# Kernel tuning notes

Hardware: AMD Instinct MI355X
Metric: run time of the kernel (lower is better)

Reference implementation:

```python
import jax, jax.numpy as jnp
import numpy as np

B, S, F, H, D = 32, 512, 32, 8, 300   # batch, seq, n_features, hidden_dim, n_dim_model
FH = min(D, F)                        # flattened GRN hidden = min(n_dim_model, n_features)


def _p(key, shape, scale=0.05):
    return (jax.random.normal(key, shape) * scale).astype(jnp.float32)


def setup_inputs() -> dict:
    key = jax.random.key(0)
    ks = jax.random.split(key, 16)
    return {
        "x": jax.random.normal(ks[0], (B, S, F), dtype=jnp.float32),
        "pre_w": _p(ks[1], (F, H)), "pre_b": _p(ks[2], (F, H)),
        "sg_fc1_w": _p(ks[3], (F, H, H)), "sg_fc1_b": _p(ks[4], (F, H)),
        "sg_fc2_w": _p(ks[5], (F, H, D)), "sg_fc2_b": _p(ks[6], (F, D)),
        "sg_gate_w": _p(ks[7], (F, D, 2 * D)), "sg_gate_b": _p(ks[8], (F, 2 * D)),
        "sg_ln_g": jnp.ones((F, D), jnp.float32), "sg_ln_b": jnp.zeros((F, D), jnp.float32),
        "fl_fc1_w": _p(ks[9], (F * H, FH)), "fl_fc1_b": _p(ks[10], (FH,)),
        "fl_fc2_w": _p(ks[11], (FH, F)), "fl_fc2_b": _p(ks[12], (F,)),
        "fl_gate_w": _p(ks[13], (F, 2 * F)), "fl_gate_b": _p(ks[14], (2 * F,)),
        "fl_ln_g": jnp.ones((F,), jnp.float32), "fl_ln_b": jnp.zeros((F,), jnp.float32),
    }


def _interp_last(x, out_dim):
    # torch F.interpolate(mode='linear', align_corners=True) along the last axis
    in_dim = x.shape[-1]
    pos = jnp.arange(out_dim) * ((in_dim - 1) / (out_dim - 1))
    lo = jnp.floor(pos).astype(jnp.int32)
    hi = jnp.minimum(lo + 1, in_dim - 1)
    w = (pos - lo.astype(pos.dtype)).astype(x.dtype)
    return x[..., lo] * (1 - w) + x[..., hi] * w


def _layer_norm(x, g, b, eps=1e-5):
    m = jnp.mean(x, axis=-1, keepdims=True)
    v = jnp.var(x, axis=-1, keepdims=True)
    return (x - m) * jax.lax.rsqrt(v + eps) * g + b


def _forward(x, pre_w, pre_b, sg_fc1_w, sg_fc1_b, sg_fc2_w, sg_fc2_b,
             sg_gate_w, sg_gate_b, sg_ln_g, sg_ln_b,
             fl_fc1_w, fl_fc1_b, fl_fc2_w, fl_fc2_b, fl_gate_w, fl_gate_b,
             fl_ln_g, fl_ln_b):
    # per-feature prescaler: Linear(1, H) for each of F features, batched
    pre = x[..., None] * pre_w + pre_b                                   # [B,S,F,H]

    # per-feature GRN (H -> H -> D), batched over the feature axis f
    h = jax.nn.elu(jnp.einsum('bsfh,fhk->bsfk', pre, sg_fc1_w) + sg_fc1_b)
    h = jnp.einsum('bsfk,fkd->bsfd', h, sg_fc2_w) + sg_fc2_b             # [B,S,F,D]
    g = jnp.einsum('bsfd,fdp->bsfp', h, sg_gate_w) + sg_gate_b           # [B,S,F,2D]
    glu = g[..., :D] * jax.nn.sigmoid(g[..., D:])
    residual = _interp_last(pre, D)                                      # H -> D interpolate projection
    outputs = _layer_norm(glu + residual, sg_ln_g, sg_ln_b)              # [B,S,F,D]

    # flattened GRN on concatenated prescaler outputs (F*H -> FH -> F)
    flat = pre.reshape(pre.shape[0], pre.shape[1], F * H)                # matches torch.cat order
    fh = jax.nn.elu(flat @ fl_fc1_w + fl_fc1_b)
    fh = fh @ fl_fc2_w + fl_fc2_b                                        # [B,S,F]
    fg = fh @ fl_gate_w + fl_gate_b                                      # [B,S,2F]
    fglu = fg[..., :F] * jax.nn.sigmoid(fg[..., F:])
    wlogits = _layer_norm(fglu + _interp_last(flat, F), fl_ln_g, fl_ln_b)
    w = jax.nn.softmax(wlogits, axis=-1)                                 # [B,S,F]

    out = jnp.einsum('bsfd,bsf->bsd', outputs, w)                        # softmax-weighted sum over features
    return out, w[..., None, :]                                          # weights unsqueezed at dim -2


def reference(x, pre_w, pre_b, sg_fc1_w, sg_fc1_b, sg_fc2_w, sg_fc2_b,
              sg_gate_w, sg_gate_b, sg_ln_g, sg_ln_b,
              fl_fc1_w, fl_fc1_b, fl_fc2_w, fl_fc2_b, fl_gate_w, fl_gate_b,
              fl_ln_g, fl_ln_b):
    return _forward(x, pre_w, pre_b, sg_fc1_w, sg_fc1_b, sg_fc2_w, sg_fc2_b,
                    sg_gate_w, sg_gate_b, sg_ln_g, sg_ln_b,
                    fl_fc1_w, fl_fc1_b, fl_fc2_w, fl_fc2_b, fl_gate_w, fl_gate_b,
                    fl_ln_g, fl_ln_b)
```

## Files before the change

### kernel.cpp

```cpp
#include <hip/hip_runtime.h>
#include <hip/hip_bf16.h>

#define NB 32
#define NS 512
#define NF 32
#define NH 8
#define ND 300
#define NTOK (NB*NS)
#define TPW 8
#define WPB 2
#define TPB (TPW*WPB)

#define L2E 1.4426950408889634f

using bf16 = __hip_bfloat16;
typedef float v2f __attribute__((ext_vector_type(2)));

__device__ __forceinline__ float rcpf_(float x){ return __builtin_amdgcn_rcpf(x); }
__device__ __forceinline__ float rsqf_(float x){ return __builtin_amdgcn_rsqf(x); }
__device__ __forceinline__ float sigm(float x){ return rcpf_(1.0f + __expf(-x)); }
__device__ __forceinline__ float sigm2(float x){ return rcpf_(1.0f + __builtin_amdgcn_exp2f(-x)); }
__device__ __forceinline__ float eluf(float x){ return x > 0.0f ? x : __expf(x) - 1.0f; }

__device__ __forceinline__ v2f fma2(v2f a, v2f b, v2f c){
    return __builtin_elementwise_fma(a, b, c);
}
__device__ __forceinline__ v2f fma2s(float s, v2f b, v2f c){
    return __builtin_elementwise_fma((v2f){s, s}, b, c);
}

template<int BF16>
__device__ __forceinline__ float ldf(const void* p, size_t i){
    if (BF16) return __bfloat162float(((const bf16*)p)[i]);
    return ((const float*)p)[i];
}
template<int BF16>
__device__ __forceinline__ void stf(void* p, size_t i, float v){
    if (BF16) ((bf16*)p)[i] = __float2bfloat16(v);
    else      ((float*)p)[i] = v;
}

__device__ __forceinline__ bool is_bf16(const void* ones){
    return *(const unsigned*)ones == 0x3F803F80u;
}

__device__ __forceinline__ v2f unpk(unsigned u){
    return (v2f){ __int_as_float((int)(u << 16)),
                  __int_as_float((int)(u & 0xFFFF0000u)) };
}
__device__ __forceinline__ unsigned pack_bf(float a, float b){
    bf16 ha = __float2bfloat16(a), hb = __float2bfloat16(b);
    return (unsigned)*(unsigned short*)&ha | ((unsigned)*(unsigned short*)&hb << 16);
}

template<int CTRL>
__device__ __forceinline__ float dppadd(float v){
    return v + __int_as_float(__builtin_amdgcn_update_dpp(
        0, __float_as_int(v), CTRL, 0xF, 0xF, true));
}
template<int CTRL>
__device__ __forceinline__ float dppmax(float v){
    return fmaxf(v, __int_as_float(__builtin_amdgcn_update_dpp(
        __float_as_int(v), __float_as_int(v), CTRL, 0xF, 0xF, false)));
}
__device__ __forceinline__ float rlane(float v, int l){
    return __int_as_float(__builtin_amdgcn_readlane(__float_as_int(v), l));
}
__device__ __forceinline__ float wsum64(float v){
    v = dppadd<0x111>(v); v = dppadd<0x112>(v); v = dppadd<0x114>(v); v = dppadd<0x118>(v);
    v = dppadd<0x142>(v); v = dppadd<0x143>(v);
    return rlane(v, 63);
}
__device__ __forceinline__ float rsum32(float v){
    v = dppadd<0x111>(v); v = dppadd<0x112>(v); v = dppadd<0x114>(v); v = dppadd<0x118>(v);
    return rlane(v, 15) + rlane(v, 31);
}
__device__ __forceinline__ float rmax32(float v){
    v = dppmax<0x111>(v); v = dppmax<0x112>(v); v = dppmax<0x114>(v); v = dppmax<0x118>(v);
    return fmaxf(rlane(v, 15), rlane(v, 31));
}

template<int BF16>
__device__ void precompute_body(const void* __restrict__ W2, const void* __restrict__ b2,
                                const void* __restrict__ Wg, const void* __restrict__ bg,
                                const void* __restrict__ sg_g, const void* __restrict__ sg_b,
                                unsigned* __restrict__ Crow,
                                float* __restrict__ w2t, float* __restrict__ b2s,
                                float (*part)[64][18])
{
    const int tid  = threadIdx.x;
    const int lane = tid & 63;
    const int wv   = tid >> 6;
    const int f    = blockIdx.x & 31;
    const int c    = blockIdx.x >> 5;
    const int d    = c * 64 + lane;
    const int dc   = d < 299 ? d : 299;

    for (int idx = tid; idx < 2400; idx += 512) {
        int m = idx >> 3, k = idx & 7;
        w2t[idx] = ldf<BF16>(W2, (size_t)f * 2400 + (size_t)k * 300 + m);
    }
    if (tid < 300) b2s[tid] = ldf<BF16>(b2, (size_t)f * 300 + tid);
    __syncthreads();

    v2f aA01 = {0,0}, aA23 = {0,0}, aA45 = {0,0}, aA67 = {0,0};
    v2f aB01 = {0,0}, aB23 = {0,0}, aB45 = {0,0}, aB67 = {0,0};
    float bAa = 0.f, bBa = 0.f;

    const int m0 = (wv * 300) >> 3;
    const int m1 = ((wv + 1) * 300) >> 3;
    const size_t WgF = (size_t)f * 180000 + dc;
    #pragma unroll 4
    for (int m = m0; m < m1; ++m) {
        float wa = ldf<BF16>(Wg, WgF + (size_t)m * 600);
        float wb = ldf<BF16>(Wg, WgF + (size_t)m * 600 + 300);
        float4 wk0 = *(const float4*)(w2t + m * 8);
        float4 wk1 = *(const float4*)(w2t + m * 8 + 4);
        aA01 = fma2s(wa, (v2f){wk0.x, wk0.y}, aA01);
        aA23 = fma2s(wa, (v2f){wk0.z, wk0.w}, aA23);
        aA45 = fma2s(wa, (v2f){wk1.x, wk1.y}, aA45);
        aA67 = fma2s(wa, (v2f){wk1.z, wk1.w}, aA67);
        aB01 = fma2s(wb, (v2f){wk0.x, wk0.y}, aB01);
        aB23 = fma2s(wb, (v2f){wk0.z, wk0.w}, aB23);
        aB45 = fma2s(wb, (v2f){wk1.x, wk1.y}, aB45);
        aB67 = fma2s(wb, (v2f){wk1.z, wk1.w}, aB67);
        float b2v = b2s[m];
        bAa += b2v * wa;
        bBa += b2v * wb;
    }

    {
        float* p = part[wv][lane];
        p[0]  = aA01.x; p[1]  = aA01.y; p[2]  = aA23.x; p[3]  = aA23.y;
        p[4]  = aA45.x; p[5]  = aA45.y; p[6]  = aA67.x; p[7]  = aA67.y;
        p[8]  = aB01.x; p[9]  = aB01.y; p[10] = aB23.x; p[11] = aB23.y;
        p[12] = aB45.x; p[13] = aB45.y; p[14] = aB67.x; p[15] = aB67.y;
        p[16] = bAa;    p[17] = bBa;
    }
    __syncthreads();

    if (tid < 64 && d < 300) {
        float s[18];
        #pragma unroll
        for (int v = 0; v < 18; ++v) {
            float t0 = part[0][lane][v] + part[1][lane][v];
            float t1 = part[2][lane][v] + part[3][lane][v];
            float t2 = part[4][lane][v] + part[5][lane][v];
            float t3 = part[6][lane][v] + part[7][lane][v];
            s[v] = (t0 + t1) + (t2 + t3);
        }
        unsigned dw[12];
        #pragma unroll
        for (int k = 0; k < 8; ++k) dw[k] = pack_bf(s[k], s[8 + k] * L2E);
        dw[8]  = __float_as_uint(s[16] + ldf<BF16>(bg, (size_t)f * 600 + d));
        dw[9]  = __float_as_uint((s[17] + ldf<BF16>(bg, (size_t)f * 600 + d + 300)) * L2E);
        dw[10] = __float_as_uint(ldf<BF16>(sg_g, (size_t)f * 300 + d));
        dw[11] = __float_as_uint(ldf<BF16>(sg_b, (size_t)f * 300 + d));
        unsigned* row = Crow + (size_t)(f * 300 + d) * 12;
        *(uint4*)(row + 0) = make_uint4(dw[0], dw[1], dw[2],  dw[3]);
        *(uint4*)(row + 4) = make_uint4(dw[4], dw[5], dw[6],  dw[7]);
        *(uint4*)(row + 8) = make_uint4(dw[8], dw[9], dw[10], dw[11]);
    }
}

__global__ void precompute_kernel(const void* __restrict__ W2, const void* __restrict__ b2,
                                  const void* __restrict__ Wg, const void* __restrict__ bg,
                                  const void* __restrict__ sg_g, const void* __restrict__ sg_b,
                                  unsigned* __restrict__ Crow)
{
    __shared__ float w2t[2400];
    __shared__ float b2s[300];
    __shared__ float part[8][64][18];
    if (is_bf16(sg_g))
        precompute_body<1>(W2, b2, Wg, bg, sg_g, sg_b, Crow, w2t, b2s, part);
    else
        precompute_body<0>(W2, b2, Wg, bg, sg_g, sg_b, Crow, w2t, b2s, part);
}

template<int BF16>
__device__ void vsn_body(const void* __restrict__ x,
                         const void* __restrict__ pre_w, const void* __restrict__ pre_b,
                         const void* __restrict__ W1,    const void* __restrict__ b1,
                         const void* __restrict__ fl1w,  const void* __restrict__ fl1b,
                         const void* __restrict__ fl2w,  const void* __restrict__ fl2b,
                         const void* __restrict__ flgw,  const void* __restrict__ flgb,
                         const void* __restrict__ flng,  const void* __restrict__ flnb,
                         const unsigned* __restrict__ Crow,
                         void* __restrict__ d_out, float* preS_, unsigned* hS_)
{
    void* outMain = d_out;
    void* outW    = (char*)d_out + (size_t)NTOK * ND * (BF16 ? 2 : 4);

    const int tid  = threadIdx.x;
    const int wave = tid >> 6;
    const int lane = tid & 63;
    const int tokBase = blockIdx.x * TPB + wave * TPW;

    float*    myPre = preS_ + wave * (TPW * 256);
    unsigned* myH   = hS_   + wave * (TPW * 128);

    {
        float pw[4], pb[4];
        #pragma unroll
        for (int q = 0; q < 4; ++q) {
            pw[q] = ldf<BF16>(pre_w, 4 * lane + q);
            pb[q] = ldf<BF16>(pre_b, 4 * lane + q);
        }
        const int fidx = lane >> 1;
        #pragma unroll
        for (int t = 0; t < TPW; ++t) {
            float xv = ldf<BF16>(x, (size_t)(tokBase + t) * NF + fidx);
            float4 v;
            v.x = xv * pw[0] + pb[0];
            v.y = xv * pw[1] + pb[1];
            v.z = xv * pw[2] + pb[2];
            v.w = xv * pw[3] + pb[3];
            *(float4*)(&myPre[t * 256 + 4 * lane]) = v;
        }
    }

    {
        const int f  = lane >> 1;
        const int kh = (lane & 1) * 4;
        float w1r[8][4], b1r[4];
        #pragma unroll
        for (int m = 0; m < 8; ++m)
            #pragma unroll
            for (int q = 0; q < 4; ++q)
                w1r[m][q] = ldf<BF16>(W1, (size_t)(f * 8 + m) * 8 + kh + q);
        #pragma unroll
        for (int q = 0; q < 4; ++q) b1r[q] = ldf<BF16>(b1, f * 8 + kh + q);

        #pragma unroll
        for (int t = 0; t < TPW; ++t) {
            float pr[8];
            float4 pA = *(const float4*)(&myPre[t * 256 + f * 8]);
            float4 pB = *(const float4*)(&myPre[t * 256 + f * 8 + 4]);
            pr[0]=pA.x; pr[1]=pA.y; pr[2]=pA.z; pr[3]=pA.w;
            pr[4]=pB.x; pr[5]=pB.y; pr[6]=pB.z; pr[7]=pB.w;
            float a[4] = {b1r[0], b1r[1], b1r[2], b1r[3]};
            #pragma unroll
            for (int m = 0; m < 8; ++m)
                #pragma unroll
                for (int q = 0; q < 4; ++q)
                    a[q] += pr[m] * w1r[m][q];
            uint2 hp;
            hp.x = pack_bf(eluf(a[0]), eluf(a[1]));
            hp.y = pack_bf(eluf(a[2]), eluf(a[3]));
            *(uint2*)(&myH[t * 128 + 2 * lane]) = hp;
        }
    }

    const int jj = lane & 31;
    const int hB = lane >> 5;
    float wreg[TPW];
    {
        float f1b = (hB == 0) ? ldf<BF16>(fl1b, jj) : 0.0f;
        v2f p1v[TPW / 2];
        #pragma unroll
        for (int g = 0; g < TPW / 2; ++g) p1v[g] = (v2f){f1b, f1b};
        for (int kg = 0; kg < 32; ++kg) {
            const int kk = hB * 128 + kg * 4;
            float4 pr[TPW];
            #pragma unroll
            for (int t = 0; t < TPW; ++t)
                pr[t] = *(const float4*)(&myPre[t * 256 + kk]);
            float w0 = ldf<BF16>(fl1w, (size_t)(kk + 0) * 32 + jj);
            float w1 = ldf<BF16>(fl1w, (size_t)(kk + 1) * 32 + jj);
            float w2 = ldf<BF16>(fl1w, (size_t)(kk + 2) * 32 + jj);
            float w3 = ldf<BF16>(fl1w, (size_t)(kk + 3) * 32 + jj);
            #pragma unroll
            for (int g = 0; g < TPW / 2; ++g) {
                p1v[g] = fma2((v2f){pr[2*g].x, pr[2*g+1].x}, (v2f){w0, w0}, p1v[g]);
                p1v[g] = fma2((v2f){pr[2*g].y, pr[2*g+1].y}, (v2f){w1, w1}, p1v[g]);
                p1v[g] = fma2((v2f){pr[2*g].z, pr[2*g+1].z}, (v2f){w2, w2}, p1v[g]);
                p1v[g] = fma2((v2f){pr[2*g].w, pr[2*g+1].w}, (v2f){w3, w3}, p1v[g]);
            }
        }
        float fhv[TPW];
        #pragma unroll
        for (int t = 0; t < TPW; ++t) {
            float p1 = (t & 1) ? p1v[t >> 1].y : p1v[t >> 1].x;
            fhv[t] = eluf(p1 + __shfl_xor(p1, 32));
        }

        float p2[TPW];
        float f2b = ldf<BF16>(fl2b, jj);
        #pragma unroll
        for (int t = 0; t < TPW; ++t) p2[t] = f2b;
        #pragma unroll
        for (int k = 0; k < 32; ++k) {
            float wv = ldf<BF16>(fl2w, k * 32 + jj);
            #pragma unroll
            for (int t = 0; t < TPW; ++t) p2[t] += rlane(fhv[t], k) * wv;
        }
        float p3[TPW];
        float fgbv = ldf<BF16>(flgb, lane);
        #pragma unroll
        for (int t = 0; t < TPW; ++t) p3[t] = fgbv;
        #pragma unroll
        for (int k = 0; k < 32; ++k) {
            float wv = ldf<BF16>(flgw, k * 64 + lane);
            #pragma unroll
            for (int t = 0; t < TPW; ++t) p3[t] += rlane(p2[t], k) * wv;
        }

        float lng = ldf<BF16>(flng, jj), lnb = ldf<BF16>(flnb, jj);
        float posB = (float)jj * (255.0f / 31.0f);
        int loB = (int)floorf(posB); loB = loB < 0 ? 0 : (loB > 254 ? 254 : loB);
        float frB = posB - (float)loB;

        #pragma unroll
        for (int t = 0; t < TPW; ++t) {
            float fgA  = __shfl(p3[t], jj);
            float fgB  = __shfl(p3[t], jj + 32);
            float fglu = fgA * sigm(fgB);
            float pl = myPre[t * 256 + loB];
            float ph = myPre[t * 256 + loB + 1];
            float tv = fglu + pl + frB * (ph - pl);
            float S1 = rsum32(tv);
            float S2 = rsum32(tv * tv);
            float mean = S1 * (1.0f / 32.0f);
            float var  = fmaxf(S2 * (1.0f / 32.0f) - mean * mean, 0.0f);
            float rs   = rsqf_(var + 1e-5f);
            float wl   = (tv - mean) * rs * lng + lnb;
            float mx   = rmax32(wl);
            float e    = __expf(wl - mx);
            float ss   = rsum32(e);
            float wv   = e * rcpf_(ss);
            wreg[t] = wv;
            if (lane < 32) stf<BF16>(outW, (size_t)(tokBase + t) * NF + lane, wv);
        }
    }

    int lo_[5]; float fr_[5];
    #pragma unroll
    for (int i = 0; i < 5; ++i) {
        int d = i * 64 + lane;
        float pos = (float)d * (7.0f / 299.0f);
        int lo = (int)floorf(pos); lo = lo < 0 ? 0 : (lo > 6 ? 6 : lo);
        lo_[i] = lo; fr_[i] = pos - (float)lo;
    }

    float acc[TPW][5];
    #pragma unroll
    for (int t = 0; t < TPW; ++t)
        #pragma unroll
        for (int i = 0; i < 5; ++i) acc[t][i] = 0.0f;

    for (int f = 0; f < NF; ++f) {
        v2f  P[5][8];
        float bcA[5], bcB[5], lgv[5], lbv[5];
        #pragma unroll
        for (int i = 0; i < 5; ++i) {
            int d = i * 64 + lane;
            bool ok = (d < ND);
            const uint4* row = (const uint4*)(Crow + ((size_t)f * ND + (ok ? d : ND - 1)) * 12);
            uint4 c0 = row[0], c1 = row[1], c2 = row[2];
            P[i][0] = unpk(c0.x); P[i][1] = unpk(c0.y);
            P[i][2] = unpk(c0.z); P[i][3] = unpk(c0.w);
            P[i][4] = unpk(c1.x); P[i][5] = unpk(c1.y);
            P[i][6] = unpk(c1.z); P[i][7] = unpk(c1.w);
            bcA[i] = __uint_as_float(c2.x);
            bcB[i] = __uint_as_float(c2.y);
            lgv[i] = __uint_as_float(c2.z);
            lbv[i] = __uint_as_float(c2.w);
        }

        #pragma unroll
        for (int t = 0; t < TPW; ++t) {
            uint4 hp = *(const uint4*)(&myH[t * 128 + f * 4]);
            v2f h01 = unpk(hp.x), h23 = unpk(hp.y), h45 = unpk(hp.z), h67 = unpk(hp.w);

            float tt[5], a1 = 0.f, a2 = 0.f;
            #pragma unroll
            for (int i = 0; i < 5; ++i) {
                int d = i * 64 + lane;
                bool ok = (d < ND);
                v2f g = {bcA[i], bcB[i]};
                g = fma2s(h01.x, P[i][0], g);
                g = fma2s(h01.y, P[i][1], g);
                g = fma2s(h23.x, P[i][2], g);
                g = fma2s(h23.y, P[i][3], g);
                g = fma2s(h45.x, P[i][4], g);
                g = fma2s(h45.y, P[i][5], g);
                g = fma2s(h67.x, P[i][6], g);
                g = fma2s(h67.y, P[i][7], g);
                int base = f * 8 + lo_[i];
                float pl = myPre[t * 256 + base];
                float ph = myPre[t * 256 + base + 1];
                float tv = g.x * sigm2(g.y) + pl + fr_[i] * (ph - pl);
                tv = ok ? tv : 0.0f;
                tt[i] = tv; a1 += tv; a2 += tv * tv;
            }

            float S1 = wsum64(a1);
            float S2 = wsum64(a2);
            float mean = S1 * (1.0f / 300.0f);
            float var  = fmaxf(S2 * (1.0f / 300.0f) - mean * mean, 0.0f);
            float rs   = rsqf_(var + 1e-5f);
            float wf   = rlane(wreg[t], f);
            float c1v  = wf * rs;
            float c2v  = -c1v * mean;
            #pragma unroll
            for (int i = 0; i < 5; ++i) {
                int d = i * 64 + lane;
                if (d < ND) {
                    float v = fmaf(c1v, tt[i], c2v);
                    acc[t][i] = fmaf(lgv[i], v, fmaf(wf, lbv[i], acc[t][i]));
                }
            }
        }
    }

    #pragma unroll
    for (int t = 0; t < TPW; ++t) {
        const size_t tok = (size_t)tokBase + t;
        #pragma unroll
        for (int i = 0; i < 5; ++i) {
            int d = i * 64 + lane;
            if (d < ND) stf<BF16>(outMain, tok * ND + d, acc[t][i]);
        }
    }
}

__launch_bounds__(128)
__global__ void vsn_main(const void* __restrict__ x,
                         const void* __restrict__ pre_w, const void* __restrict__ pre_b,
                         const void* __restrict__ W1,    const void* __restrict__ b1,
                         const void* __restrict__ fl1w,  const void* __restrict__ fl1b,
                         const void* __restrict__ fl2w,  const void* __restrict__ fl2b,
                         const void* __restrict__ flgw,  const void* __restrict__ flgb,
                         const void* __restrict__ flng,  const void* __restrict__ flnb,
                         const unsigned* __restrict__ Crow, void* __restrict__ d_out)
{
    __shared__ float    preS_[WPB * TPW * 256];
    __shared__ unsigned hS_[WPB * TPW * 128];
    if (is_bf16(flng))
        vsn_body<1>(x, pre_w, pre_b, W1, b1, fl1w, fl1b, fl2w, fl2b,
                    flgw, flgb, flng, flnb, Crow, d_out, preS_, hS_);
    else
        vsn_body<0>(x, pre_w, pre_b, W1, b1, fl1w, fl1b, fl2w, fl2b,
                    flgw, flgb, flng, flnb, Crow, d_out, preS_, hS_);
}

extern "C" void kernel_launch(void* const* d_in, const int* in_sizes, int n_in,
                              void* d_out, int out_size, void* d_ws, size_t ws_size,
                              hipStream_t stream)
{
    const void* x     = d_in[0];
    const void* pre_w = d_in[1];
    const void* pre_b = d_in[2];
    const void* W1    = d_in[3];
    const void* b1    = d_in[4];
    const void* W2    = d_in[5];
    const void* b2    = d_in[6];
    const void* Wg    = d_in[7];
    const void* bg    = d_in[8];
    const void* sg_g  = d_in[9];
    const void* sg_b  = d_in[10];
    const void* fl1w  = d_in[11];
    const void* fl1b  = d_in[12];
    const void* fl2w  = d_in[13];
    const void* fl2b  = d_in[14];
    const void* flgw  = d_in[15];
    const void* flgb  = d_in[16];
    const void* flng  = d_in[17];
    const void* flnb  = d_in[18];

    unsigned* Crow = (unsigned*)d_ws;

    precompute_kernel<<<160, 512, 0, stream>>>(W2, b2, Wg, bg, sg_g, sg_b, Crow);

    vsn_main<<<NTOK / TPB, 128, 0, stream>>>(x, pre_w, pre_b, W1, b1,
        fl1w, fl1b, fl2w, fl2b, flgw, flgb, flng, flnb, Crow, d_out);
}
```

Before: 303.1 us.

## Split feature loop across waves per token block and precompute interpolated prescaler residual

Result: slower. 344.3 us (+13.6%).

```diff
diff --git a/kernel.cpp b/kernel.cpp
--- a/kernel.cpp
+++ b/kernel.cpp
@@ -9,7 +9,7 @@
 #define NTOK (NB*NS)
 #define TPW 8
 #define WPB 2
-#define TPB (TPW*WPB)
+#define TPB 8
 
 #define L2E 1.4426950408889634f
 
@@ -84,6 +84,7 @@
 __device__ void precompute_body(const void* __restrict__ W2, const void* __restrict__ b2,
                                 const void* __restrict__ Wg, const void* __restrict__ bg,
                                 const void* __restrict__ sg_g, const void* __restrict__ sg_b,
+                                const void* __restrict__ pre_w, const void* __restrict__ pre_b,
                                 unsigned* __restrict__ Crow,
                                 float* __restrict__ w2t, float* __restrict__ b2s,
                                 float (*part)[64][18])
@@ -156,25 +157,38 @@
         dw[9]  = __float_as_uint((s[17] + ldf<BF16>(bg, (size_t)f * 600 + d + 300)) * L2E);
         dw[10] = __float_as_uint(ldf<BF16>(sg_g, (size_t)f * 300 + d));
         dw[11] = __float_as_uint(ldf<BF16>(sg_b, (size_t)f * 300 + d));
-        unsigned* row = Crow + (size_t)(f * 300 + d) * 12;
-        *(uint4*)(row + 0) = make_uint4(dw[0], dw[1], dw[2],  dw[3]);
-        *(uint4*)(row + 4) = make_uint4(dw[4], dw[5], dw[6],  dw[7]);
-        *(uint4*)(row + 8) = make_uint4(dw[8], dw[9], dw[10], dw[11]);
+
+        float pos = (float)d * (7.0f / 299.0f);
+        int lo = (int)floorf(pos); lo = lo < 0 ? 0 : (lo > 6 ? 6 : lo);
+        float fr = pos - (float)lo;
+        float pwl = ldf<BF16>(pre_w, (size_t)f * 8 + lo);
+        float pwh = ldf<BF16>(pre_w, (size_t)f * 8 + lo + 1);
+        float pbl = ldf<BF16>(pre_b, (size_t)f * 8 + lo);
+        float pbh = ldf<BF16>(pre_b, (size_t)f * 8 + lo + 1);
+        unsigned rwu = __float_as_uint(pwl + fr * (pwh - pwl));
+        unsigned rbu = __float_as_uint(pbl + fr * (pbh - pbl));
+
+        unsigned* row = Crow + (size_t)(f * 300 + d) * 16;
+        *(uint4*)(row + 0)  = make_uint4(dw[0], dw[1], dw[2],  dw[3]);
+        *(uint4*)(row + 4)  = make_uint4(dw[4], dw[5], dw[6],  dw[7]);
+        *(uint4*)(row + 8)  = make_uint4(dw[8], dw[9], dw[10], dw[11]);
+        *(uint4*)(row + 12) = make_uint4(rwu, rbu, 0u, 0u);
     }
 }
 
 __global__ void precompute_kernel(const void* __restrict__ W2, const void* __restrict__ b2,
                                   const void* __restrict__ Wg, const void* __restrict__ bg,
                                   const void* __restrict__ sg_g, const void* __restrict__ sg_b,
+                                  const void* __restrict__ pre_w, const void* __restrict__ pre_b,
                                   unsigned* __restrict__ Crow)
 {
     __shared__ float w2t[2400];
     __shared__ float b2s[300];
     __shared__ float part[8][64][18];
     if (is_bf16(sg_g))
-        precompute_body<1>(W2, b2, Wg, bg, sg_g, sg_b, Crow, w2t, b2s, part);
+        precompute_body<1>(W2, b2, Wg, bg, sg_g, sg_b, pre_w, pre_b, Crow, w2t, b2s, part);
     else
-        precompute_body<0>(W2, b2, Wg, bg, sg_g, sg_b, Crow, w2t, b2s, part);
+        precompute_body<0>(W2, b2, Wg, bg, sg_g, sg_b, pre_w, pre_b, Crow, w2t, b2s, part);
 }
 
 template<int BF16>
@@ -186,18 +200,23 @@
                          const void* __restrict__ flgw,  const void* __restrict__ flgb,
                          const void* __restrict__ flng,  const void* __restrict__ flnb,
                          const unsigned* __restrict__ Crow,
-                         void* __restrict__ d_out, float* preS_, unsigned* hS_)
+                         void* __restrict__ d_out, float* preS, unsigned* hS)
 {
     void* outMain = d_out;
     void* outW    = (char*)d_out + (size_t)NTOK * ND * (BF16 ? 2 : 4);
 
-    const int tid  = threadIdx.x;
-    const int wave = tid >> 6;
-    const int lane = tid & 63;
-    const int tokBase = blockIdx.x * TPB + wave * TPW;
-
-    float*    myPre = preS_ + wave * (TPW * 256);
-    unsigned* myH   = hS_   + wave * (TPW * 128);
+    const int tid   = threadIdx.x;
+    const int wave  = tid >> 6;
+    const int lane  = tid & 63;
+    const int tokBase = blockIdx.x * TPB;
+    const int tA0   = wave * (TPB / WPB);
+    const int fBase = wave * (NF / WPB);
+
+    {
+    }
+    const int tx = lane & 7, fo = lane >> 3;
+    float xrA = ldf<BF16>(x, (size_t)(tokBase + tx) * NF + fBase + fo);
+    float xrB = ldf<BF16>(x, (size_t)(tokBase + tx) * NF + fBase + 8 + fo);
 
     {
         float pw[4], pb[4];
@@ -208,14 +227,15 @@
         }
         const int fidx = lane >> 1;
         #pragma unroll
-        for (int t = 0; t < TPW; ++t) {
+        for (int j = 0; j < TPB / WPB; ++j) {
+            int t = tA0 + j;
             float xv = ldf<BF16>(x, (size_t)(tokBase + t) * NF + fidx);
             float4 v;
             v.x = xv * pw[0] + pb[0];
             v.y = xv * pw[1] + pb[1];
             v.z = xv * pw[2] + pb[2];
             v.w = xv * pw[3] + pb[3];
-            *(float4*)(&myPre[t * 256 + 4 * lane]) = v;
+            *(float4*)(&preS[t * 256 + 4 * lane]) = v;
         }
     }
 
@@ -232,10 +252,11 @@
         for (int q = 0; q < 4; ++q) b1r[q] = ldf<BF16>(b1, f * 8 + kh + q);
 
         #pragma unroll
-        for (int t = 0; t < TPW; ++t) {
+        for (int j = 0; j < TPB / WPB; ++j) {
+            int t = tA0 + j;
             float pr[8];
-            float4 pA = *(const float4*)(&myPre[t * 256 + f * 8]);
-            float4 pB = *(const float4*)(&myPre[t * 256 + f * 8 + 4]);
+            float4 pA = *(const float4*)(&preS[t * 256 + f * 8]);
+            float4 pB = *(const float4*)(&preS[t * 256 + f * 8 + 4]);
             pr[0]=pA.x; pr[1]=pA.y; pr[2]=pA.z; pr[3]=pA.w;
             pr[4]=pB.x; pr[5]=pB.y; pr[6]=pB.z; pr[7]=pB.w;
             float a[4] = {b1r[0], b1r[1], b1r[2], b1r[3]};
@@ -247,9 +268,10 @@
             uint2 hp;
             hp.x = pack_bf(eluf(a[0]), eluf(a[1]));
             hp.y = pack_bf(eluf(a[2]), eluf(a[3]));
-            *(uint2*)(&myH[t * 128 + 2 * lane]) = hp;
-        }
-    }
+            *(uint2*)(&hS[t * 128 + 2 * lane]) = hp;
+        }
+    }
+    __syncthreads();
 
     const int jj = lane & 31;
     const int hB = lane >> 5;
@@ -264,7 +286,7 @@
             float4 pr[TPW];
             #pragma unroll
             for (int t = 0; t < TPW; ++t)
-                pr[t] = *(const float4*)(&myPre[t * 256 + kk]);
+                pr[t] = *(const float4*)(&preS[t * 256 + kk]);
             float w0 = ldf<BF16>(fl1w, (size_t)(kk + 0) * 32 + jj);
             float w1 = ldf<BF16>(fl1w, (size_t)(kk + 1) * 32 + jj);
             float w2 = ldf<BF16>(fl1w, (size_t)(kk + 2) * 32 + jj);
@@ -315,8 +337,8 @@
             float fgA  = __shfl(p3[t], jj);
             float fgB  = __shfl(p3[t], jj + 32);
             float fglu = fgA * sigm(fgB);
-            float pl = myPre[t * 256 + loB];
-            float ph = myPre[t * 256 + loB + 1];
+            float pl = preS[t * 256 + loB];
+            float ph = preS[t * 256 + loB + 1];
             float tv = fglu + pl + frB * (ph - pl);
             float S1 = rsum32(tv);
             float S2 = rsum32(tv * tv);
@@ -329,17 +351,8 @@
             float ss   = rsum32(e);
             float wv   = e * rcpf_(ss);
             wreg[t] = wv;
-            if (lane < 32) stf<BF16>(outW, (size_t)(tokBase + t) * NF + lane, wv);
-        }
-    }
-
-    int lo_[5]; float fr_[5];
-    #pragma unroll
-    for (int i = 0; i < 5; ++i) {
-        int d = i * 64 + lane;
-        float pos = (float)d * (7.0f / 299.0f);
-        int lo = (int)floorf(pos); lo = lo < 0 ? 0 : (lo > 6 ? 6 : lo);
-        lo_[i] = lo; fr_[i] = pos - (float)lo;
+            if (wave == 0 && lane < 32) stf<BF16>(outW, (size_t)(tokBase + t) * NF + lane, wv);
+        }
     }
 
     float acc[TPW][5];
@@ -348,15 +361,19 @@
         #pragma unroll
         for (int i = 0; i < 5; ++i) acc[t][i] = 0.0f;
 
-    for (int f = 0; f < NF; ++f) {
+    for (int fi = 0; fi < NF / WPB; ++fi) {
+        const int f = fBase + fi;
         v2f  P[5][8];
-        float bcA[5], bcB[5], lgv[5], lbv[5];
+        float bcA[5], bcB[5], lgv[5], lbv[5], rwv[5], rbv[5];
         #pragma unroll
         for (int i = 0; i < 5; ++i) {
             int d = i * 64 + lane;
-            bool ok = (d < ND);
-            const uint4* row = (const uint4*)(Crow + ((size_t)f * ND + (ok ? d : ND - 1)) * 12);
-            uint4 c0 = row[0], c1 = row[1], c2 = row[2];
+            int dcl = d < ND ? d : ND - 1;
+            const unsigned* rp = Crow + ((size_t)f * ND + dcl) * 16;
+            uint4 c0 = *(const uint4*)(rp + 0);
+            uint4 c1 = *(const uint4*)(rp + 4);
+            uint4 c2 = *(const uint4*)(rp + 8);
+            uint2 c3 = *(const uint2*)(rp + 12);
             P[i][0] = unpk(c0.x); P[i][1] = unpk(c0.y);
             P[i][2] = unpk(c0.z); P[i][3] = unpk(c0.w);
             P[i][4] = unpk(c1.x); P[i][5] = unpk(c1.y);
@@ -365,12 +382,17 @@
             bcB[i] = __uint_as_float(c2.y);
             lgv[i] = __uint_as_float(c2.z);
             lbv[i] = __uint_as_float(c2.w);
-        }
+            rwv[i] = __uint_as_float(c3.x);
+            rbv[i] = __uint_as_float(c3.y);
+        }
+
+        float xq = (fi < 8) ? xrA : xrB;
 
         #pragma unroll
         for (int t = 0; t < TPW; ++t) {
-            uint4 hp = *(const uint4*)(&myH[t * 128 + f * 4]);
+            uint4 hp = *(const uint4*)(&hS[t * 128 + f * 4]);
             v2f h01 = unpk(hp.x), h23 = unpk(hp.y), h45 = unpk(hp.z), h67 = unpk(hp.w);
+            float xv = rlane(xq, ((fi & 7) << 3) | t);
 
             float tt[5], a1 = 0.f, a2 = 0.f;
             #pragma unroll
@@ -386,12 +408,9 @@
                 g = fma2s(h45.y, P[i][5], g);
                 g = fma2s(h67.x, P[i][6], g);
                 g = fma2s(h67.y, P[i][7], g);
-                int base = f * 8 + lo_[i];
-                float pl = myPre[t * 256 + base];
-                float ph = myPre[t * 256 + base + 1];
-                float tv = g.x * sigm2(g.y) + pl + fr_[i] * (ph - pl);
+                float tv = fmaf(xv, rwv[i], rbv[i]) + g.x * sigm2(g.y);
                 tv = ok ? tv : 0.0f;
-                tt[i] = tv; a1 += tv; a2 += tv * tv;
+                tt[i] = tv; a1 += tv; a2 = fmaf(tv, tv, a2);
             }
 
             float S1 = wsum64(a1);
@@ -413,13 +432,25 @@
         }
     }
 
-    #pragma unroll
-    for (int t = 0; t < TPW; ++t) {
-        const size_t tok = (size_t)tokBase + t;
-        #pragma unroll
-        for (int i = 0; i < 5; ++i) {
-            int d = i * 64 + lane;
-            if (d < ND) stf<BF16>(outMain, tok * ND + d, acc[t][i]);
+    __syncthreads();
+    if (wave == 0) {
+        #pragma unroll
+        for (int t = 0; t < TPW; ++t)
+            #pragma unroll
+            for (int i = 0; i < 5; ++i)
+                preS[(t * 5 + i) * 64 + lane] = acc[t][i];
+    }
+    __syncthreads();
+    if (wave == 1) {
+        #pragma unroll
+        for (int t = 0; t < TPW; ++t) {
+            const size_t tok = (size_t)tokBase + t;
+            #pragma unroll
+            for (int i = 0; i < 5; ++i) {
+                int d = i * 64 + lane;
+                if (d < ND)
+                    stf<BF16>(outMain, tok * ND + d, acc[t][i] + preS[(t * 5 + i) * 64 + lane]);
+            }
         }
     }
 }
@@ -434,8 +465,8 @@
                          const void* __restrict__ flng,  const void* __restrict__ flnb,
                          const unsigned* __restrict__ Crow, void* __restrict__ d_out)
 {
-    __shared__ float    preS_[WPB * TPW * 256];
-    __shared__ unsigned hS_[WPB * TPW * 128];
+    __shared__ float    preS_[2560];
+    __shared__ unsigned hS_[TPB * 128];
     if (is_bf16(flng))
         vsn_body<1>(x, pre_w, pre_b, W1, b1, fl1w, fl1b, fl2w, fl2b,
                     flgw, flgb, flng, flnb, Crow, d_out, preS_, hS_);
@@ -470,7 +501,8 @@
 
     unsigned* Crow = (unsigned*)d_ws;
 
-    precompute_kernel<<<160, 512, 0, stream>>>(W2, b2, Wg, bg, sg_g, sg_b, Crow);
+    precompute_kernel<<<160, 512, 0, stream>>>(W2, b2, Wg, bg, sg_g, sg_b,
+                                               pre_w, pre_b, Crow);
 
     vsn_main<<<NTOK / TPB, 128, 0, stream>>>(x, pre_w, pre_b, W1, b1,
         fl1w, fl1b, fl2w, fl2b, flgw, flgb, flng, flnb, Crow, d_out);
```
